# Kernel optimization log

Hardware: AMD Instinct MI355X
Metric: run time of the kernel (lower is better)

## Reference

```python
import jax, jax.numpy as jnp
import numpy as np

L, H, D, V, T, B = 12, 12, 768, 50257, 1024, 2
HD = D // H


def _ln(x, w, b):
    m = jnp.mean(x, axis=-1, keepdims=True)
    v = jnp.var(x, axis=-1, keepdims=True)
    return (x - m) * jax.lax.rsqrt(v + 1e-5) * w + b


def setup_inputs() -> dict:
    key = jax.random.key(0)
    ks = jax.random.split(key, 8)
    def n(k, shape, std=0.02):
        return jax.random.normal(k, shape, jnp.float32) * std
    return dict(
        x=jax.random.randint(ks[0], (B, T), 0, V),
        wte=n(ks[1], (V, D), 0.01),
        wpe=n(ks[2], (T, D), 0.01),
        ln1_w=jnp.ones((L, D), jnp.float32), ln1_b=jnp.zeros((L, D), jnp.float32),
        qkv_w=n(ks[3], (L, D, 3 * D)), qkv_b=jnp.zeros((L, 3 * D), jnp.float32),
        proj_w=n(ks[4], (L, D, D)), proj_b=jnp.zeros((L, D), jnp.float32),
        ln2_w=jnp.ones((L, D), jnp.float32), ln2_b=jnp.zeros((L, D), jnp.float32),
        fc_w=n(ks[5], (L, D, 4 * D)), fc_b=jnp.zeros((L, 4 * D), jnp.float32),
        fcp_w=n(ks[6], (L, 4 * D, D)), fcp_b=jnp.zeros((L, D), jnp.float32),
        lnf_w=jnp.ones((D,), jnp.float32), lnf_b=jnp.zeros((D,), jnp.float32),
    )


def reference(x, wte, wpe, ln1_w, ln1_b, qkv_w, qkv_b, proj_w, proj_b,
              ln2_w, ln2_b, fc_w, fc_b, fcp_w, fcp_b, lnf_w, lnf_b):
    Bn, Tn = x.shape
    h = wte[x] + wpe[:Tn]                                   # [B,T,D]
    mask = jnp.tril(jnp.ones((Tn, Tn), bool))               # causal mask
    scale = 1.0 / np.sqrt(HD).astype(np.float32)

    def block(h, p):
        l1w, l1b, qw, qb, pw, pb, l2w, l2b, fw, fb, p2w, p2b = p
        a = _ln(h, l1w, l1b)
        qkv = a @ qw + qb                                    # [B,T,3D]
        q, k, v = jnp.split(qkv, 3, axis=-1)
        q = q.reshape(Bn, Tn, H, HD)
        k = k.reshape(Bn, Tn, H, HD)
        v = v.reshape(Bn, Tn, H, HD)
        att = jnp.einsum('bqhd,bkhd->bhqk', q, k) * scale    # [B,H,T,T]
        att = jnp.where(mask, att, -jnp.inf)
        att = jax.nn.softmax(att, axis=-1)
        y = jnp.einsum('bhqk,bkhd->bqhd', att, v).reshape(Bn, Tn, D)
        h = h + y @ pw + pb
        m = _ln(h, l2w, l2b)
        m = jax.nn.gelu(m @ fw + fb, approximate=True)       # tanh GELU
        h = h + m @ p2w + p2b
        return h, None

    h, _ = jax.lax.scan(block, h, (ln1_w, ln1_b, qkv_w, qkv_b, proj_w, proj_b,
                                   ln2_w, ln2_b, fc_w, fc_b, fcp_w, fcp_b))
    logits = _ln(h, lnf_w, lnf_b) @ wte.T                    # tied lm_head
    return logits
```

## Files before the change

kernel.cpp:

```cpp
#include <hip/hip_runtime.h>
#include <hip/hip_bf16.h>

typedef __hip_bfloat16 hbf16;
using bf16x8 = __attribute__((ext_vector_type(8))) __bf16;
using f32x4 = __attribute__((ext_vector_type(4))) float;

constexpr int Lc = 12, Hc = 12, Dc = 768, Vc = 50257, Tc = 1024, Bc = 2, HDc = 64;
constexpr int Mc = Bc * Tc;
constexpr int Vpad = 50304;

constexpr size_t SZ_Q = (size_t)3 * Dc * Dc;
constexpr size_t SZ_P = (size_t)Dc * Dc;
constexpr size_t SZ_F = (size_t)4 * Dc * Dc;
constexpr size_t SZ_FP = (size_t)4 * Dc * Dc;
constexpr size_t SZL = SZ_Q + SZ_P + SZ_F + SZ_FP;

#define GLD16(gp, lp)                                               \
    __builtin_amdgcn_global_load_lds(                               \
        (__attribute__((address_space(1))) void*)(void*)(gp),       \
        (__attribute__((address_space(3))) void*)(void*)(lp), 16, 0, 0)

__global__ void embed_kernel(const int* __restrict__ x, const float* __restrict__ wte,
                             const float* __restrict__ wpe, float* __restrict__ h) {
    int i = blockIdx.x * blockDim.x + threadIdx.x;
    if (i >= Mc * Dc) return;
    int m = i / Dc, d = i - m * Dc;
    int t = m % Tc;
    int tok = x[m];
    h[i] = wte[(size_t)tok * Dc + d] + wpe[(size_t)t * Dc + d];
}

__global__ __launch_bounds__(256) void ln_kernel(const float* __restrict__ x,
                                                 const float* __restrict__ w,
                                                 const float* __restrict__ b,
                                                 hbf16* __restrict__ out) {
    int wv = threadIdx.x >> 6, lane = threadIdx.x & 63;
    int row = blockIdx.x * 4 + wv;
    const float4* xr = (const float4*)(x + (size_t)row * Dc);
    float4 v[3];
    float s = 0.f, sq = 0.f;
#pragma unroll
    for (int i = 0; i < 3; i++) {
        v[i] = xr[i * 64 + lane];
        s += v[i].x + v[i].y + v[i].z + v[i].w;
        sq += v[i].x * v[i].x + v[i].y * v[i].y + v[i].z * v[i].z + v[i].w * v[i].w;
    }
#pragma unroll
    for (int o = 32; o > 0; o >>= 1) {
        s += __shfl_xor(s, o, 64);
        sq += __shfl_xor(sq, o, 64);
    }
    float mean = s * (1.f / Dc);
    float var = sq * (1.f / Dc) - mean * mean;
    float rstd = rsqrtf(var + 1e-5f);
#pragma unroll
    for (int i = 0; i < 3; i++) {
        int c = (i * 64 + lane) * 4;
        float4 wv4 = *(const float4*)(w + c);
        float4 bv4 = *(const float4*)(b + c);
        float r0 = (v[i].x - mean) * rstd * wv4.x + bv4.x;
        float r1 = (v[i].y - mean) * rstd * wv4.y + bv4.y;
        float r2 = (v[i].z - mean) * rstd * wv4.z + bv4.z;
        float r3 = (v[i].w - mean) * rstd * wv4.w + bv4.w;
        __bf16 q0 = (__bf16)r0, q1 = (__bf16)r1, q2 = (__bf16)r2, q3 = (__bf16)r3;
        ushort4 u;
        u.x = *(unsigned short*)&q0; u.y = *(unsigned short*)&q1;
        u.z = *(unsigned short*)&q2; u.w = *(unsigned short*)&q3;
        *(ushort4*)(out + (size_t)row * Dc + c) = u;
    }
}

__global__ __launch_bounds__(256) void transpose4_kernel(
    const float* __restrict__ s0, const float* __restrict__ s1,
    const float* __restrict__ s2, const float* __restrict__ s3,
    hbf16* __restrict__ d0, hbf16* __restrict__ d1,
    hbf16* __restrict__ d2, hbf16* __restrict__ d3) {
    int id = blockIdx.x;
    size_t lz = blockIdx.y;
    int bx, by, K, N;
    const float* W;
    hbf16* Wt;
    if (id < 1728)      { int t = id;        bx = t % 72; by = t / 72; K = 768;  N = 2304; W = s0 + lz * SZ_Q;  Wt = d0 + lz * SZL; }
    else if (id < 2304) { int t = id - 1728; bx = t % 24; by = t / 24; K = 768;  N = 768;  W = s1 + lz * SZ_P;  Wt = d1 + lz * SZL; }
    else if (id < 4608) { int t = id - 2304; bx = t % 96; by = t / 96; K = 768;  N = 3072; W = s2 + lz * SZ_F;  Wt = d2 + lz * SZL; }
    else                { int t = id - 4608; bx = t % 24; by = t / 24; K = 3072; N = 768;  W = s3 + lz * SZ_FP; Wt = d3 + lz * SZL; }

    __shared__ float tile[32][33];
    int n0 = bx * 32, k0 = by * 32;
    int tx = threadIdx.x & 31, ty = threadIdx.x >> 5;
#pragma unroll
    for (int i = 0; i < 4; i++) {
        int r = ty + i * 8;
        tile[r][tx] = W[(size_t)(k0 + r) * N + n0 + tx];
    }
    __syncthreads();
#pragma unroll
    for (int i = 0; i < 4; i++) {
        int r = ty + i * 8;
        Wt[(size_t)(n0 + r) * K + k0 + tx] = __float2bfloat16(tile[tx][r]);
    }
}

__global__ void convert_wte(const float* __restrict__ wte, hbf16* __restrict__ out) {
    size_t i4 = ((size_t)blockIdx.x * 256 + threadIdx.x) * 4;
    if (i4 >= (size_t)Vpad * Dc) return;
    if (i4 < (size_t)Vc * Dc) {
#pragma unroll
        for (int j = 0; j < 4; j++) out[i4 + j] = __float2bfloat16(wte[i4 + j]);
    } else {
#pragma unroll
        for (int j = 0; j < 4; j++) out[i4 + j] = __float2bfloat16(0.f);
    }
}

template <int EPI, bool OUTBF, int BN>
__global__ __launch_bounds__(256) void mm_kernel(const hbf16* __restrict__ A,
                                                 const hbf16* __restrict__ Bt,
                                                 const float* __restrict__ bias,
                                                 const float* __restrict__ resid,
                                                 void* __restrict__ Cout,
                                                 int M, int N, int K) {
    constexpr int NF = BN / 32;
    constexpr int NBI = BN / 32;
    __shared__ __bf16 As[2][128 * 64];
    __shared__ __bf16 Bs[2][BN * 64];
    int tid = threadIdx.x;
    int l = tid & 63, w = tid >> 6;
    int wr = w >> 1, wc = w & 1;

    int gx = gridDim.x, gy = gridDim.y;
    int nwg = gx * gy;
    int hwlin = blockIdx.y * gx + blockIdx.x;
    int wk = (hwlin & 7) * (nwg >> 3) + (hwlin >> 3);
    int m0 = (wk % gy) * 128;
    int n0 = (wk / gy) * BN;

    int sr = tid >> 3, sc = tid & 7;
    int scs = (sc ^ (sr & 7)) * 8;
    const hbf16* pA[4];
#pragma unroll
    for (int j = 0; j < 4; j++) pA[j] = A + (size_t)(m0 + j * 32 + sr) * K + scs;
    const hbf16* pB[NBI];
#pragma unroll
    for (int j = 0; j < NBI; j++) pB[j] = Bt + (size_t)(n0 + j * 32 + sr) * K + scs;

    auto stage = [&](int bi, int ko) {
#pragma unroll
        for (int j = 0; j < 4; j++) GLD16(pA[j] + ko, &As[bi][j * 2048 + tid * 8]);
#pragma unroll
        for (int j = 0; j < NBI; j++) GLD16(pB[j] + ko, &Bs[bi][j * 2048 + tid * 8]);
    };

    int lr = l & 15, lg = l >> 4;
    int aoff[2][4], boff[2][NF];
#pragma unroll
    for (int kk = 0; kk < 2; kk++) {
        int ks = ((kk * 4 + lg) ^ (lr & 7)) * 8;
#pragma unroll
        for (int m = 0; m < 4; m++) aoff[kk][m] = (wr * 64 + m * 16 + lr) * 64 + ks;
#pragma unroll
        for (int n = 0; n < NF; n++) boff[kk][n] = (wc * (BN / 2) + n * 16 + lr) * 64 + ks;
    }

    f32x4 acc[4][NF] = {};
    int nk = K / 64;

    stage(0, 0);
    for (int t = 0; t < nk; ++t) {
        int cur = t & 1;
        if (t + 1 < nk) {
            stage(cur ^ 1, (t + 1) * 64);
            if constexpr (BN == 128)
                asm volatile("s_waitcnt vmcnt(8)" ::: "memory");
            else
                asm volatile("s_waitcnt vmcnt(6)" ::: "memory");
        } else {
            asm volatile("s_waitcnt vmcnt(0)" ::: "memory");
        }
        __builtin_amdgcn_sched_barrier(0);
        __builtin_amdgcn_s_barrier();
        __builtin_amdgcn_sched_barrier(0);
#pragma unroll
        for (int kk = 0; kk < 2; kk++) {
            bf16x8 af[4], bfr[NF];
#pragma unroll
            for (int m = 0; m < 4; m++) af[m] = *(const bf16x8*)&As[cur][aoff[kk][m]];
#pragma unroll
            for (int n = 0; n < NF; n++) bfr[n] = *(const bf16x8*)&Bs[cur][boff[kk][n]];
#pragma unroll
            for (int m = 0; m < 4; m++)
#pragma unroll
                for (int n = 0; n < NF; n++)
                    acc[m][n] = __builtin_amdgcn_mfma_f32_16x16x32_bf16(af[m], bfr[n], acc[m][n], 0, 0, 0);
        }
        __builtin_amdgcn_s_barrier();
    }

#pragma unroll
    for (int n = 0; n < NF; n++) {
        int col = n0 + wc * (BN / 2) + n * 16 + lr;
        bool cok = col < N;
        float bv = (bias && cok) ? bias[col] : 0.f;
#pragma unroll
        for (int m = 0; m < 4; m++) {
#pragma unroll
            for (int r = 0; r < 4; r++) {
                int row = m0 + wr * 64 + m * 16 + lg * 4 + r;
                if (!cok) continue;
                float v = acc[m][n][r] + bv;
                if (EPI == 1) v += resid[(size_t)row * N + col];
                if (EPI == 2) {
                    float x3 = v * v * v;
                    v = 0.5f * v * (1.f + tanhf(0.7978845608028654f * (v + 0.044715f * x3)));
                }
                if (OUTBF)
                    ((hbf16*)Cout)[(size_t)row * N + col] = __float2bfloat16(v);
                else
                    ((float*)Cout)[(size_t)row * N + col] = v;
            }
        }
    }
}

__global__ __launch_bounds__(512) void mm2_kernel(const hbf16* __restrict__ A,
                                                  const hbf16* __restrict__ Bt,
                                                  float* __restrict__ Cout,
                                                  int M, int N, int K) {
    __shared__ __bf16 As[256 * 64];
    __shared__ __bf16 Bs[128 * 64];
    int tid = threadIdx.x;
    int l = tid & 63, w = tid >> 6;
    int wr = w >> 1, wc = w & 1;

    int gx = gridDim.x, gy = gridDim.y;
    int nwg = gx * gy;
    int hwlin = blockIdx.y * gx + blockIdx.x;
    int wk = (hwlin & 7) * (nwg >> 3) + (hwlin >> 3);
    int m0 = (wk & 7) * 256;
    int n0 = (wk >> 3) * 128;

    int sr = tid >> 3, sc = tid & 7;
    int scs = (sc ^ (sr & 7)) * 8;
    const hbf16* pA[4];
    __bf16* lA[4];
#pragma unroll
    for (int j = 0; j < 4; j++) {
        pA[j] = A + (size_t)(m0 + j * 64 + sr) * K + scs;
        lA[j] = As + j * 4096 + tid * 8;
    }
    const hbf16* pB[2];
    __bf16* lB[2];
#pragma unroll
    for (int j = 0; j < 2; j++) {
        pB[j] = Bt + (size_t)(n0 + j * 64 + sr) * K + scs;
        lB[j] = Bs + j * 4096 + tid * 8;
    }

    int lr = l & 15, lg = l >> 4;
    int aoff[2][4], boff[2][4];
#pragma unroll
    for (int kk = 0; kk < 2; kk++) {
        int ks = ((kk * 4 + lg) ^ (lr & 7)) * 8;
#pragma unroll
        for (int m = 0; m < 4; m++) aoff[kk][m] = (wr * 64 + m * 16 + lr) * 64 + ks;
#pragma unroll
        for (int n = 0; n < 4; n++) boff[kk][n] = (wc * 64 + n * 16 + lr) * 64 + ks;
    }

    f32x4 acc[4][4] = {};

    for (int k0 = 0; k0 < K; k0 += 64) {
#pragma unroll
        for (int j = 0; j < 4; j++) {
            GLD16(pA[j], lA[j]);
            pA[j] += 64;
        }
#pragma unroll
        for (int j = 0; j < 2; j++) {
            GLD16(pB[j], lB[j]);
            pB[j] += 64;
        }
        __syncthreads();
#pragma unroll
        for (int kk = 0; kk < 2; kk++) {
            bf16x8 af[4], bfr[4];
#pragma unroll
            for (int m = 0; m < 4; m++) af[m] = *(const bf16x8*)&As[aoff[kk][m]];
#pragma unroll
            for (int n = 0; n < 4; n++) bfr[n] = *(const bf16x8*)&Bs[boff[kk][n]];
#pragma unroll
            for (int m = 0; m < 4; m++)
#pragma unroll
                for (int n = 0; n < 4; n++)
                    acc[m][n] = __builtin_amdgcn_mfma_f32_16x16x32_bf16(af[m], bfr[n], acc[m][n], 0, 0, 0);
        }
        __syncthreads();
    }

#pragma unroll
    for (int n = 0; n < 4; n++) {
        int col = n0 + wc * 64 + n * 16 + lr;
        if (col >= N) continue;
#pragma unroll
        for (int m = 0; m < 4; m++) {
#pragma unroll
            for (int r = 0; r < 4; r++) {
                int row = m0 + wr * 64 + m * 16 + lg * 4 + r;
                Cout[(size_t)row * N + col] = acc[m][n][r];
            }
        }
    }
}

__global__ __launch_bounds__(256) void fattn_kernel(const hbf16* __restrict__ qkv,
                                                    hbf16* __restrict__ y) {
    int qt = gridDim.x - 1 - blockIdx.x;
    int h = blockIdx.y, b = blockIdx.z;
    int q0 = qt * 64;
    int tid = threadIdx.x;
    int l = tid & 63, w = tid >> 6;
    int li = l & 15, lg = l >> 4;
    constexpr int RS = 3 * Dc;
    constexpr int PST = 72;
    constexpr int VST = 72;
    constexpr float SCL = 0.125f * 1.44269504f;
    constexpr float THR = 11.5f;

    __shared__ __bf16 K_lds[2][64 * 64];
    __shared__ __bf16 Vt[2][64 * VST];
    __shared__ __bf16 P_lds[4][16 * PST];

    bf16x8 qf[2];
    {
        const hbf16* qp = qkv + (size_t)(b * Tc + q0 + w * 16 + li) * RS + h * HDc + lg * 8;
        qf[0] = *(const bf16x8*)qp;
        qf[1] = *(const bf16x8*)(qp + 32);
    }

    int krow0 = tid >> 3, krow1 = 32 + (tid >> 3);
    int ks8 = tid & 7;
    int kc0 = (ks8 ^ (krow0 & 7)) * 8;
    int kc1 = (ks8 ^ (krow1 & 7)) * 8;
    const hbf16* kbase = qkv + (size_t)(b * Tc) * RS + Dc + h * HDc;

    int jp = (tid >> 3) * 2;
    int db = (tid & 7) * 8;
    const hbf16* vbase = qkv + (size_t)(b * Tc) * RS + 2 * Dc + h * HDc;

    int koff[2][4];
#pragma unroll
    for (int ks = 0; ks < 2; ks++)
#pragma unroll
        for (int n = 0; n < 4; n++)
            koff[ks][n] = (n * 16 + li) * 64 + (((ks * 4 + lg) ^ (li & 7)) * 8);

    f32x4 acc_o[4] = {};
    float m_run = -1e30f, l_run = 0.f;

    bf16x8 vr0, vr1;
    {
        const hbf16* vp = vbase + (size_t)jp * RS + db;
        vr0 = *(const bf16x8*)vp;
        vr1 = *(const bf16x8*)(vp + RS);
        GLD16(kbase + (size_t)krow0 * RS + kc0, &K_lds[0][tid * 8]);
        GLD16(kbase + (size_t)krow1 * RS + kc1, &K_lds[0][2048 + tid * 8]);
    }
#pragma unroll
    for (int i = 0; i < 8; i++) {
        __bf16 a0 = vr0[i], a1 = vr1[i];
        unsigned u = (unsigned)*(unsigned short*)&a0 | ((unsigned)*(unsigned short*)&a1 << 16);
        *(unsigned*)&Vt[0][(db + i) * VST + jp] = u;
    }

    int cur = 0;
    for (int jt = 0; jt <= qt; jt++) {
        int jn0 = (jt < qt) ? (jt + 1) * 64 : 0;

        asm volatile("s_waitcnt lgkmcnt(0)" ::: "memory");
        __builtin_amdgcn_s_barrier();

        {
            const hbf16* vp = vbase + (size_t)(jn0 + jp) * RS + db;
            vr0 = *(const bf16x8*)vp;
            vr1 = *(const bf16x8*)(vp + RS);
            GLD16(kbase + (size_t)(jn0 + krow0) * RS + kc0, &K_lds[cur ^ 1][tid * 8]);
            GLD16(kbase + (size_t)(jn0 + krow1) * RS + kc1, &K_lds[cur ^ 1][2048 + tid * 8]);
        }

        asm volatile("s_waitcnt vmcnt(4)" ::: "memory");
        __builtin_amdgcn_sched_barrier(0);

        f32x4 s[4] = {};
#pragma unroll
        for (int ks = 0; ks < 2; ks++)
#pragma unroll
            for (int n = 0; n < 4; n++) {
                bf16x8 kf = *(const bf16x8*)&K_lds[cur][koff[ks][n]];
                s[n] = __builtin_amdgcn_mfma_f32_16x16x32_bf16(kf, qf[ks], s[n], 0, 0, 0);
            }
#pragma unroll
        for (int n = 0; n < 4; n++)
#pragma unroll
            for (int r = 0; r < 4; r++) s[n][r] *= SCL;

        if (jt == qt) {
            int qloc = w * 16 + li;
#pragma unroll
            for (int n = 0; n < 4; n++)
#pragma unroll
                for (int r = 0; r < 4; r++)
                    if (n * 16 + lg * 4 + r > qloc) s[n][r] = -1e30f;
        }

        float mx = -1e30f;
#pragma unroll
        for (int n = 0; n < 4; n++)
#pragma unroll
            for (int r = 0; r < 4; r++) mx = fmaxf(mx, s[n][r]);
        mx = fmaxf(mx, __shfl_xor(mx, 16, 64));
        mx = fmaxf(mx, __shfl_xor(mx, 32, 64));

        bool dfr = __all(mx - m_run <= THR);
        float sclq = 1.f;
        if (!dfr) {
            float mnew = fmaxf(m_run, mx);
            sclq = exp2f(m_run - mnew);
            m_run = mnew;
        }
        float rs = 0.f;
#pragma unroll
        for (int n = 0; n < 4; n++)
#pragma unroll
            for (int r = 0; r < 4; r++) {
                float pv = exp2f(s[n][r] - m_run);
                s[n][r] = pv;
                rs += pv;
            }
        rs += __shfl_xor(rs, 16, 64);
        rs += __shfl_xor(rs, 32, 64);
        l_run = (dfr ? l_run : l_run * sclq) + rs;

#pragma unroll
        for (int n = 0; n < 4; n++)
#pragma unroll
            for (int r = 0; r < 4; r += 2) {
                __bf16 b0 = (__bf16)s[n][r], b1 = (__bf16)s[n][r + 1];
                unsigned u = (unsigned)*(unsigned short*)&b0 |
                             ((unsigned)*(unsigned short*)&b1 << 16);
                *(unsigned*)&P_lds[w][li * PST + n * 16 + lg * 4 + r] = u;
            }
        bf16x8 pa0 = *(const bf16x8*)&P_lds[w][li * PST + lg * 8];
        bf16x8 pa1 = *(const bf16x8*)&P_lds[w][li * PST + 32 + lg * 8];

        if (!dfr) {
#pragma unroll
            for (int r = 0; r < 4; r++) {
                float sr_ = __shfl(sclq, (l & 48) | (lg * 4 + r), 64);
#pragma unroll
                for (int n2 = 0; n2 < 4; n2++) acc_o[n2][r] *= sr_;
            }
        }

#pragma unroll
        for (int n2 = 0; n2 < 4; n2++) {
            bf16x8 vf0 = *(const bf16x8*)&Vt[cur][(n2 * 16 + li) * VST + lg * 8];
            bf16x8 vf1 = *(const bf16x8*)&Vt[cur][(n2 * 16 + li) * VST + 32 + lg * 8];
            acc_o[n2] = __builtin_amdgcn_mfma_f32_16x16x32_bf16(pa0, vf0, acc_o[n2], 0, 0, 0);
            acc_o[n2] = __builtin_amdgcn_mfma_f32_16x16x32_bf16(pa1, vf1, acc_o[n2], 0, 0, 0);
        }

#pragma unroll
        for (int i = 0; i < 8; i++) {
            __bf16 a0 = vr0[i], a1 = vr1[i];
            unsigned u = (unsigned)*(unsigned short*)&a0 | ((unsigned)*(unsigned short*)&a1 << 16);
            *(unsigned*)&Vt[cur ^ 1][(db + i) * VST + jp] = u;
        }
        cur ^= 1;
    }

#pragma unroll
    for (int r = 0; r < 4; r++) {
        float lv = __shfl(l_run, (l & 48) | (lg * 4 + r), 64);
        float rcp = 1.f / lv;
        int row = q0 + w * 16 + lg * 4 + r;
#pragma unroll
        for (int n2 = 0; n2 < 4; n2++)
            y[(size_t)(b * Tc + row) * Dc + h * HDc + n2 * 16 + li] =
                __float2bfloat16(acc_o[n2][r] * rcp);
    }
}

extern "C" void kernel_launch(void* const* d_in, const int* in_sizes, int n_in,
                              void* d_out, int out_size, void* d_ws, size_t ws_size,
                              hipStream_t stream) {
    const int* x = (const int*)d_in[0];
    const float* wte = (const float*)d_in[1];
    const float* wpe = (const float*)d_in[2];
    const float* ln1w = (const float*)d_in[3];
    const float* ln1b = (const float*)d_in[4];
    const float* qkvw = (const float*)d_in[5];
    const float* qkvb = (const float*)d_in[6];
    const float* projw = (const float*)d_in[7];
    const float* projb = (const float*)d_in[8];
    const float* ln2w = (const float*)d_in[9];
    const float* ln2b = (const float*)d_in[10];
    const float* fcw = (const float*)d_in[11];
    const float* fcb = (const float*)d_in[12];
    const float* fcpw = (const float*)d_in[13];
    const float* fcpb = (const float*)d_in[14];
    const float* lnfw = (const float*)d_in[15];
    const float* lnfb = (const float*)d_in[16];

    char* p = (char*)d_ws;
    float* h = (float*)p;     p += (size_t)Mc * Dc * 4;
    hbf16* qkv = (hbf16*)p;   p += (size_t)Mc * 3 * Dc * 2;
    hbf16* a = (hbf16*)p;     p += (size_t)Mc * Dc * 2;
    hbf16* y = (hbf16*)p;     p += (size_t)Mc * Dc * 2;
    hbf16* mlp = (hbf16*)p;   p += (size_t)Mc * 4 * Dc * 2;
    hbf16* wte_b = (hbf16*)p; p += (size_t)Vpad * Dc * 2;
    hbf16* wtr = (hbf16*)p;
    size_t used = (size_t)((char*)wtr - (char*)d_ws);
    bool all_mode = (ws_size - used) >= (size_t)Lc * SZL * 2;

    embed_kernel<<<(Mc * Dc + 255) / 256, 256, 0, stream>>>(x, wte, wpe, h);
    convert_wte<<<((size_t)Vpad * Dc / 4 + 255) / 256, 256, 0, stream>>>(wte, wte_b);

    if (all_mode) {
        transpose4_kernel<<<dim3(6912, Lc), 256, 0, stream>>>(
            qkvw, projw, fcw, fcpw,
            wtr, wtr + SZ_Q, wtr + SZ_Q + SZ_P, wtr + SZ_Q + SZ_P + SZ_F);
    }

    for (int l = 0; l < Lc; l++) {
        hbf16* base = wtr + (all_mode ? (size_t)l * SZL : 0);
        hbf16* wq_t = base;
        hbf16* wp_t = base + SZ_Q;
        hbf16* wf_t = base + SZ_Q + SZ_P;
        hbf16* wfp_t = base + SZ_Q + SZ_P + SZ_F;
        if (!all_mode) {
            transpose4_kernel<<<dim3(6912, 1), 256, 0, stream>>>(
                qkvw + (size_t)l * SZ_Q, projw + (size_t)l * SZ_P,
                fcw + (size_t)l * SZ_F, fcpw + (size_t)l * SZ_FP,
                wq_t, wp_t, wf_t, wfp_t);
        }

        ln_kernel<<<Mc / 4, 256, 0, stream>>>(h, ln1w + (size_t)l * Dc, ln1b + (size_t)l * Dc, a);
        mm_kernel<0, true, 128><<<dim3(3 * Dc / 128, Mc / 128), 256, 0, stream>>>(
            a, wq_t, qkvb + (size_t)l * 3 * Dc, nullptr, qkv, Mc, 3 * Dc, Dc);
        fattn_kernel<<<dim3(Tc / 64, Hc, Bc), 256, 0, stream>>>(qkv, y);
        mm_kernel<1, false, 64><<<dim3(Dc / 64, Mc / 128), 256, 0, stream>>>(
            y, wp_t, projb + (size_t)l * Dc, h, h, Mc, Dc, Dc);
        ln_kernel<<<Mc / 4, 256, 0, stream>>>(h, ln2w + (size_t)l * Dc, ln2b + (size_t)l * Dc, a);
        mm_kernel<2, true, 128><<<dim3(4 * Dc / 128, Mc / 128), 256, 0, stream>>>(
            a, wf_t, fcb + (size_t)l * 4 * Dc, nullptr, mlp, Mc, 4 * Dc, Dc);
        mm_kernel<1, false, 64><<<dim3(Dc / 64, Mc / 128), 256, 0, stream>>>(
            mlp, wfp_t, fcpb + (size_t)l * Dc, h, h, Mc, Dc, 4 * Dc);
    }

    ln_kernel<<<Mc / 4, 256, 0, stream>>>(h, lnfw, lnfb, a);
    mm2_kernel<<<dim3(Vpad / 128, Mc / 256), 512, 0, stream>>>(
        a, wte_b, (float*)d_out, Mc, Vc, Dc);
}
```

Measured before the change: 2.255 ms.

## Split long causal attention query tiles across two KV halves with merge kernel

The attention kernel now launches 24 blocks per (batch, head) instead of 16. The eight longest causal query tiles (8 to 15) are each split into two blocks that process the lower and upper halves of their key range. Those split blocks write unnormalized fp32 partial outputs plus per-row running max and sum to workspace, and a new merge kernel combines them with log-sum-exp rescaling. The aim is to shorten the critical path set by the longest causal tiles and to balance work across CUs. The cost is an extra kernel launch per layer, fp32 partial-output traffic, and additional workspace.

```diff
diff --git a/kernel.cpp b/kernel.cpp
--- a/kernel.cpp
+++ b/kernel.cpp
@@ -14,6 +14,7 @@
 constexpr size_t SZ_F = (size_t)4 * Dc * Dc;
 constexpr size_t SZ_FP = (size_t)4 * Dc * Dc;
 constexpr size_t SZL = SZ_Q + SZ_P + SZ_F + SZ_FP;
+constexpr int NPART = Bc * Hc * 8 * 2;
 
 #define GLD16(gp, lp)                                               \
     __builtin_amdgcn_global_load_lds(                               \
@@ -313,9 +314,27 @@
 }
 
 __global__ __launch_bounds__(256) void fattn_kernel(const hbf16* __restrict__ qkv,
-                                                    hbf16* __restrict__ y) {
-    int qt = gridDim.x - 1 - blockIdx.x;
+                                                    hbf16* __restrict__ y,
+                                                    float* __restrict__ part_O,
+                                                    float* __restrict__ part_m,
+                                                    float* __restrict__ part_l) {
+    int s = blockIdx.x;
     int h = blockIdx.y, b = blockIdx.z;
+    int qt, jlo, jhi, half = 0;
+    bool partial;
+    if (s < 16) {
+        qt = 8 + (s >> 1);
+        half = s & 1;
+        int mid = (qt + 1) >> 1;
+        jlo = half ? mid : 0;
+        jhi = half ? qt : mid - 1;
+        partial = true;
+    } else {
+        qt = s - 16;
+        jlo = 0;
+        jhi = qt;
+        partial = false;
+    }
     int q0 = qt * 64;
     int tid = threadIdx.x;
     int l = tid & 63, w = tid >> 6;
@@ -357,13 +376,14 @@
     f32x4 acc_o[4] = {};
     float m_run = -1e30f, l_run = 0.f;
 
+    int j0p = jlo * 64;
     bf16x8 vr0, vr1;
     {
-        const hbf16* vp = vbase + (size_t)jp * RS + db;
+        const hbf16* vp = vbase + (size_t)(j0p + jp) * RS + db;
         vr0 = *(const bf16x8*)vp;
         vr1 = *(const bf16x8*)(vp + RS);
-        GLD16(kbase + (size_t)krow0 * RS + kc0, &K_lds[0][tid * 8]);
-        GLD16(kbase + (size_t)krow1 * RS + kc1, &K_lds[0][2048 + tid * 8]);
+        GLD16(kbase + (size_t)(j0p + krow0) * RS + kc0, &K_lds[0][tid * 8]);
+        GLD16(kbase + (size_t)(j0p + krow1) * RS + kc1, &K_lds[0][2048 + tid * 8]);
     }
 #pragma unroll
     for (int i = 0; i < 8; i++) {
@@ -373,8 +393,8 @@
     }
 
     int cur = 0;
-    for (int jt = 0; jt <= qt; jt++) {
-        int jn0 = (jt < qt) ? (jt + 1) * 64 : 0;
+    for (int jt = jlo; jt <= jhi; jt++) {
+        int jn0 = (jt < jhi) ? (jt + 1) * 64 : j0p;
 
         asm volatile("s_waitcnt lgkmcnt(0)" ::: "memory");
         __builtin_amdgcn_s_barrier();
@@ -390,18 +410,18 @@
         asm volatile("s_waitcnt vmcnt(4)" ::: "memory");
         __builtin_amdgcn_sched_barrier(0);
 
-        f32x4 s[4] = {};
+        f32x4 sv[4] = {};
 #pragma unroll
         for (int ks = 0; ks < 2; ks++)
 #pragma unroll
             for (int n = 0; n < 4; n++) {
                 bf16x8 kf = *(const bf16x8*)&K_lds[cur][koff[ks][n]];
-                s[n] = __builtin_amdgcn_mfma_f32_16x16x32_bf16(kf, qf[ks], s[n], 0, 0, 0);
+                sv[n] = __builtin_amdgcn_mfma_f32_16x16x32_bf16(kf, qf[ks], sv[n], 0, 0, 0);
             }
 #pragma unroll
         for (int n = 0; n < 4; n++)
 #pragma unroll
-            for (int r = 0; r < 4; r++) s[n][r] *= SCL;
+            for (int r = 0; r < 4; r++) sv[n][r] *= SCL;
 
         if (jt == qt) {
             int qloc = w * 16 + li;
@@ -409,14 +429,14 @@
             for (int n = 0; n < 4; n++)
 #pragma unroll
                 for (int r = 0; r < 4; r++)
-                    if (n * 16 + lg * 4 + r > qloc) s[n][r] = -1e30f;
+                    if (n * 16 + lg * 4 + r > qloc) sv[n][r] = -1e30f;
         }
 
         float mx = -1e30f;
 #pragma unroll
         for (int n = 0; n < 4; n++)
 #pragma unroll
-            for (int r = 0; r < 4; r++) mx = fmaxf(mx, s[n][r]);
+            for (int r = 0; r < 4; r++) mx = fmaxf(mx, sv[n][r]);
         mx = fmaxf(mx, __shfl_xor(mx, 16, 64));
         mx = fmaxf(mx, __shfl_xor(mx, 32, 64));
 
@@ -432,8 +452,8 @@
         for (int n = 0; n < 4; n++)
 #pragma unroll
             for (int r = 0; r < 4; r++) {
-                float pv = exp2f(s[n][r] - m_run);
-                s[n][r] = pv;
+                float pv = exp2f(sv[n][r] - m_run);
+                sv[n][r] = pv;
                 rs += pv;
             }
         rs += __shfl_xor(rs, 16, 64);
@@ -444,7 +464,7 @@
         for (int n = 0; n < 4; n++)
 #pragma unroll
             for (int r = 0; r < 4; r += 2) {
-                __bf16 b0 = (__bf16)s[n][r], b1 = (__bf16)s[n][r + 1];
+                __bf16 b0 = (__bf16)sv[n][r], b1 = (__bf16)sv[n][r + 1];
                 unsigned u = (unsigned)*(unsigned short*)&b0 |
                              ((unsigned)*(unsigned short*)&b1 << 16);
                 *(unsigned*)&P_lds[w][li * PST + n * 16 + lg * 4 + r] = u;
@@ -478,16 +498,54 @@
         cur ^= 1;
     }
 
-#pragma unroll
-    for (int r = 0; r < 4; r++) {
-        float lv = __shfl(l_run, (l & 48) | (lg * 4 + r), 64);
-        float rcp = 1.f / lv;
-        int row = q0 + w * 16 + lg * 4 + r;
-#pragma unroll
-        for (int n2 = 0; n2 < 4; n2++)
-            y[(size_t)(b * Tc + row) * Dc + h * HDc + n2 * 16 + li] =
-                __float2bfloat16(acc_o[n2][r] * rcp);
-    }
+    if (partial) {
+        int p = ((b * Hc + h) * 8 + (qt - 8)) * 2 + half;
+#pragma unroll
+        for (int r = 0; r < 4; r++) {
+            int lrow = w * 16 + lg * 4 + r;
+#pragma unroll
+            for (int n2 = 0; n2 < 4; n2++)
+                part_O[(size_t)p * 4096 + lrow * 64 + n2 * 16 + li] = acc_o[n2][r];
+        }
+        if (lg == 0) {
+            part_m[p * 64 + w * 16 + li] = m_run;
+            part_l[p * 64 + w * 16 + li] = l_run;
+        }
+    } else {
+#pragma unroll
+        for (int r = 0; r < 4; r++) {
+            float lv = __shfl(l_run, (l & 48) | (lg * 4 + r), 64);
+            float rcp = 1.f / lv;
+            int row = q0 + w * 16 + lg * 4 + r;
+#pragma unroll
+            for (int n2 = 0; n2 < 4; n2++)
+                y[(size_t)(b * Tc + row) * Dc + h * HDc + n2 * 16 + li] =
+                    __float2bfloat16(acc_o[n2][r] * rcp);
+        }
+    }
+}
+
+__global__ __launch_bounds__(256) void fmerge_kernel(const float* __restrict__ part_O,
+                                                     const float* __restrict__ part_m,
+                                                     const float* __restrict__ part_l,
+                                                     hbf16* __restrict__ y) {
+    int gi = blockIdx.x * 4 + (threadIdx.x >> 6);
+    int lane = threadIdx.x & 63;
+    int row512 = gi & 511;
+    int bh = gi >> 9;
+    int b = bh / Hc, h = bh % Hc;
+    int qt8 = row512 >> 6, lrow = row512 & 63;
+    int p0 = (bh * 8 + qt8) * 2, p1 = p0 + 1;
+    float m0 = part_m[p0 * 64 + lrow], m1 = part_m[p1 * 64 + lrow];
+    float l0 = part_l[p0 * 64 + lrow], l1 = part_l[p1 * 64 + lrow];
+    float m = fmaxf(m0, m1);
+    float a0 = exp2f(m0 - m), a1 = exp2f(m1 - m);
+    float lsum = l0 * a0 + l1 * a1;
+    float o0 = part_O[(size_t)p0 * 4096 + lrow * 64 + lane];
+    float o1 = part_O[(size_t)p1 * 4096 + lrow * 64 + lane];
+    float o = (o0 * a0 + o1 * a1) / lsum;
+    int q = (8 + qt8) * 64 + lrow;
+    y[((size_t)b * Tc + q) * Dc + h * HDc + lane] = __float2bfloat16(o);
 }
 
 extern "C" void kernel_launch(void* const* d_in, const int* in_sizes, int n_in,
@@ -512,12 +570,15 @@
     const float* lnfb = (const float*)d_in[16];
 
     char* p = (char*)d_ws;
-    float* h = (float*)p;     p += (size_t)Mc * Dc * 4;
-    hbf16* qkv = (hbf16*)p;   p += (size_t)Mc * 3 * Dc * 2;
-    hbf16* a = (hbf16*)p;     p += (size_t)Mc * Dc * 2;
-    hbf16* y = (hbf16*)p;     p += (size_t)Mc * Dc * 2;
-    hbf16* mlp = (hbf16*)p;   p += (size_t)Mc * 4 * Dc * 2;
-    hbf16* wte_b = (hbf16*)p; p += (size_t)Vpad * Dc * 2;
+    float* h = (float*)p;      p += (size_t)Mc * Dc * 4;
+    hbf16* qkv = (hbf16*)p;    p += (size_t)Mc * 3 * Dc * 2;
+    hbf16* a = (hbf16*)p;      p += (size_t)Mc * Dc * 2;
+    hbf16* y = (hbf16*)p;      p += (size_t)Mc * Dc * 2;
+    hbf16* mlp = (hbf16*)p;    p += (size_t)Mc * 4 * Dc * 2;
+    hbf16* wte_b = (hbf16*)p;  p += (size_t)Vpad * Dc * 2;
+    float* part_O = (float*)p; p += (size_t)NPART * 4096 * 4;
+    float* part_m = (float*)p; p += (size_t)NPART * 64 * 4;
+    float* part_l = (float*)p; p += (size_t)NPART * 64 * 4;
     hbf16* wtr = (hbf16*)p;
     size_t used = (size_t)((char*)wtr - (char*)d_ws);
     bool all_mode = (ws_size - used) >= (size_t)Lc * SZL * 2;
@@ -547,7 +608,8 @@
         ln_kernel<<<Mc / 4, 256, 0, stream>>>(h, ln1w + (size_t)l * Dc, ln1b + (size_t)l * Dc, a);
         mm_kernel<0, true, 128><<<dim3(3 * Dc / 128, Mc / 128), 256, 0, stream>>>(
             a, wq_t, qkvb + (size_t)l * 3 * Dc, nullptr, qkv, Mc, 3 * Dc, Dc);
-        fattn_kernel<<<dim3(Tc / 64, Hc, Bc), 256, 0, stream>>>(qkv, y);
+        fattn_kernel<<<dim3(24, Hc, Bc), 256, 0, stream>>>(qkv, y, part_O, part_m, part_l);
+        fmerge_kernel<<<Bc * Hc * 512 / 4, 256, 0, stream>>>(part_O, part_m, part_l, y);
         mm_kernel<1, false, 64><<<dim3(Dc / 64, Mc / 128), 256, 0, stream>>>(
             y, wp_t, projb + (size_t)l * Dc, h, h, Mc, Dc, Dc);
         ln_kernel<<<Mc / 4, 256, 0, stream>>>(h, ln2w + (size_t)l * Dc, ln2b + (size_t)l * Dc, a);
```

Result: faster. 2.205 ms (-2.2%).
